# Kernel optimization log

Hardware: AMD Instinct MI355X
Metric: run time of the kernel (lower is better)

Reference implementation:

```python
import jax, jax.numpy as jnp
import numpy as np

T, N, F, H, E = 12, 10000, 32, 64, 320000


def setup_inputs() -> dict:
    key = jax.random.key(0)
    ks = jax.random.split(key, 6)
    x = jax.random.normal(ks[0], (T, N, F), dtype=jnp.float32)
    edge_index = jax.random.randint(ks[1], (2, E), 0, N, dtype=jnp.int64)
    edge_weight = jax.random.uniform(ks[2], (E,), dtype=jnp.float32)
    missing_mask = jnp.ones((T, N, F), dtype=jnp.bool_)
    # GCNConv params (Glorot-ish init); PyG lin: out = x @ W, bias added after aggregation
    W1 = jax.random.normal(ks[3], (F, H), dtype=jnp.float32) * (1.0 / np.sqrt(F))
    b1 = jnp.zeros((H,), dtype=jnp.float32)
    W2 = jax.random.normal(ks[4], (H, F), dtype=jnp.float32) * (1.0 / np.sqrt(H))
    b2 = jnp.zeros((F,), dtype=jnp.float32)
    return dict(x=x, edge_index=edge_index, edge_weight=edge_weight,
                missing_mask=missing_mask, W1=W1, b1=b1, W2=W2, b2=b2)


def _gcn_norm(edge_weight, row, col, n_nodes):
    # PyG gcn_norm with add_self_loops=False: deg from dst, sym normalization
    deg = jax.ops.segment_sum(edge_weight, col, num_segments=n_nodes)
    dinv = jnp.where(deg > 0, 1.0 / jnp.sqrt(jnp.maximum(deg, 1e-12)), 0.0)
    return dinv[row] * edge_weight * dinv[col]


def _gcn_layer(h, row, col, norm, W, b):
    # h: (T, N, Fin) -> (T, N, Fout). Gather at src, weight, scatter-add at dst.
    h = h @ W                                   # (T, N, Fout)
    msg = h[:, row, :] * norm[None, :, None]    # (T, E, Fout)
    out = jnp.zeros((h.shape[0], h.shape[1], h.shape[2]), h.dtype)
    out = out.at[:, col, :].add(msg)
    return out + b


def reference(x, edge_index, edge_weight, missing_mask, W1, b1, W2, b2):
    n_nodes = x.shape[1]
    row, col = edge_index[0], edge_index[1]
    norm = _gcn_norm(edge_weight, row, col, n_nodes)
    h = _gcn_layer(x, row, col, norm, W1, b1)   # layer 0
    h = jax.nn.relu(h)                          # relu between layers
    h = _gcn_layer(h, row, col, norm, W2, b2)   # layer 1 (out_dim = in_dim)
    return jnp.tanh(h)                          # original returns (x, 0); we return x
```

## Files before the change

### kernel.cpp

```cpp
#include <hip/hip_runtime.h>
#include <hip/hip_fp16.h>

#define T_DIM   12
#define N_NODES 10000
#define F_IN    32
#define H_DIM   64
#define NCH     3
#define TC      4
#define CHROW   (TC * F_IN)
#define NGRP    (N_NODES / 16)
#define NTASK   (NCH * NGRP)
#define NROWS   (NCH * N_NODES * TC)
#define MROWS   128

__global__ void zero_kernel(uint4* __restrict__ p, int n16) {
    int i = blockIdx.x * blockDim.x + threadIdx.x;
    if (i < n16) p[i] = make_uint4(0, 0, 0, 0);
}

__global__ void deg_hist_conv_kernel(const int* __restrict__ col,
                                     const float* __restrict__ w,
                                     float* __restrict__ deg,
                                     int* __restrict__ cnt, int E, int eb,
                                     const float* __restrict__ x,
                                     __half* __restrict__ xh) {
    int b = blockIdx.x;
    if (b < eb) {
        int e = b * 256 + threadIdx.x;
        if (e >= E) return;
        int c = col[e];
        atomicAdd(&deg[c], w[e]);
        atomicAdd(&cnt[c], 1);
    } else {
        int task = (b - eb) * 4 + (threadIdx.x >> 6);
        if (task >= NTASK) return;
        int l  = threadIdx.x & 63;
        int ch = task / NGRP;
        int ng = task - ch * NGRP;
        int n  = ng * 16 + (l >> 2);
        int t  = ch * TC + (l & 3);
        const float4* xp = (const float4*)(x + ((size_t)t * N_NODES + n) * F_IN);
        union { uint32_t u[16]; uint4 q[4]; } pk;
#pragma unroll
        for (int i = 0; i < 8; i++) {
            float4 v = xp[i];
            __half2 h0 = __floats2half2_rn(v.x, v.y);
            __half2 h1 = __floats2half2_rn(v.z, v.w);
            pk.u[2 * i]     = *(uint32_t*)&h0;
            pk.u[2 * i + 1] = *(uint32_t*)&h1;
        }
        uint4* dp = (uint4*)(xh + ((size_t)ch * N_NODES * TC + ng * 64 + l) * F_IN);
#pragma unroll
        for (int i = 0; i < 4; i++) dp[i] = pk.q[i];
    }
}

__global__ __launch_bounds__(1024) void scan_kernel(const int* __restrict__ cnt,
                                                    int* __restrict__ rowptr,
                                                    int* __restrict__ cur, int n) {
    __shared__ int part[1024];
    int tid = threadIdx.x;
    const int per = (n + 1023) / 1024;
    int base = tid * per;
    int s = 0;
    for (int i = 0; i < per; i++) {
        int idx = base + i;
        if (idx < n) s += cnt[idx];
    }
    part[tid] = s;
    __syncthreads();
    for (int off = 1; off < 1024; off <<= 1) {
        int v = 0;
        if (tid >= off) v = part[tid - off];
        __syncthreads();
        if (tid >= off) part[tid] += v;
        __syncthreads();
    }
    int run = (tid == 0) ? 0 : part[tid - 1];
    for (int i = 0; i < per; i++) {
        int idx = base + i;
        if (idx < n) { rowptr[idx] = run; cur[idx] = run; run += cnt[idx]; }
    }
    if (tid == 1023) rowptr[n] = part[1023];
}

__global__ void fill_kernel(const int* __restrict__ row,
                            const int* __restrict__ col,
                            const float* __restrict__ w,
                            const float* __restrict__ deg,
                            int* __restrict__ cur,
                            int2* __restrict__ edge_s, int E) {
    int e = blockIdx.x * blockDim.x + threadIdx.x;
    if (e >= E) return;
    int r = row[e];
    int c = col[e];
    float dr = deg[r];
    float dc = deg[c];
    float ir = dr > 0.f ? 1.0f / sqrtf(fmaxf(dr, 1e-12f)) : 0.f;
    float ic = dc > 0.f ? 1.0f / sqrtf(fmaxf(dc, 1e-12f)) : 0.f;
    float nw = ir * w[e] * ic;
    int pos = atomicAdd(&cur[c], 1);
    edge_s[pos] = make_int2(r, __float_as_int(nw));
}

__global__ __launch_bounds__(256) void gather_sp_kernel(const int* __restrict__ rowptr,
                                                        const int2* __restrict__ edge_s,
                                                        const __half* __restrict__ yh,
                                                        float* __restrict__ outp, int n) {
    int c = blockIdx.x * 8 + (threadIdx.x >> 5);
    if (c >= n) return;
    int l = threadIdx.x & 31;

    int beg = rowptr[c], end = rowptr[c + 1];
    const __half* base = yh + 4 * l;
    const size_t cstep = (size_t)N_NODES * CHROW;

    float4 a0 = {0.f, 0.f, 0.f, 0.f};
    float4 a1 = {0.f, 0.f, 0.f, 0.f};
    float4 a2 = {0.f, 0.f, 0.f, 0.f};

#pragma unroll 4
    for (int e = beg; e < end; e++) {
        int2 ed = edge_s[e];
        float nw = __int_as_float(ed.y);
        const __half* p = base + (size_t)ed.x * CHROW;
        uint2 u0 = *(const uint2*)(p);
        uint2 u1 = *(const uint2*)(p + cstep);
        uint2 u2 = *(const uint2*)(p + 2 * cstep);
        float2 f00 = __half22float2(*(__half2*)&u0.x), f01 = __half22float2(*(__half2*)&u0.y);
        float2 f10 = __half22float2(*(__half2*)&u1.x), f11 = __half22float2(*(__half2*)&u1.y);
        float2 f20 = __half22float2(*(__half2*)&u2.x), f21 = __half22float2(*(__half2*)&u2.y);
        a0.x = fmaf(f00.x, nw, a0.x); a0.y = fmaf(f00.y, nw, a0.y);
        a0.z = fmaf(f01.x, nw, a0.z); a0.w = fmaf(f01.y, nw, a0.w);
        a1.x = fmaf(f10.x, nw, a1.x); a1.y = fmaf(f10.y, nw, a1.y);
        a1.z = fmaf(f11.x, nw, a1.z); a1.w = fmaf(f11.y, nw, a1.w);
        a2.x = fmaf(f20.x, nw, a2.x); a2.y = fmaf(f20.y, nw, a2.y);
        a2.z = fmaf(f21.x, nw, a2.z); a2.w = fmaf(f21.y, nw, a2.w);
    }

    float* op = outp + (size_t)c * CHROW + 4 * l;
    const size_t ostep = (size_t)N_NODES * CHROW;
    *(float4*)(op)             = a0;
    *(float4*)(op + ostep)     = a1;
    *(float4*)(op + 2 * ostep) = a2;
}

__global__ __launch_bounds__(256) void gather_ch_kernel(const int* __restrict__ rowptr,
                                                        const int2* __restrict__ edge_s,
                                                        const __half* __restrict__ yh,
                                                        const float* __restrict__ bias,
                                                        float* __restrict__ outp, int n) {
    int c = blockIdx.x * 8 + (threadIdx.x >> 5);
    if (c >= n) return;
    int l = threadIdx.x & 31;

    int beg = rowptr[c], end = rowptr[c + 1];
    float4 b4 = *(const float4*)(bias + 4 * (l & 7));

#pragma unroll
    for (int ch = 0; ch < NCH; ch++) {
        const __half* base = yh + (size_t)ch * N_NODES * CHROW + 4 * l;
        float4 a = {0.f, 0.f, 0.f, 0.f};
#pragma unroll 8
        for (int e = beg; e < end; e++) {
            int2 ed = edge_s[e];
            float nw = __int_as_float(ed.y);
            uint2 u = *(const uint2*)(base + (size_t)ed.x * CHROW);
            float2 f0 = __half22float2(*(__half2*)&u.x);
            float2 f1 = __half22float2(*(__half2*)&u.y);
            a.x = fmaf(f0.x, nw, a.x);
            a.y = fmaf(f0.y, nw, a.y);
            a.z = fmaf(f1.x, nw, a.z);
            a.w = fmaf(f1.y, nw, a.w);
        }
        a.x = tanhf(a.x + b4.x); a.y = tanhf(a.y + b4.y);
        a.z = tanhf(a.z + b4.z); a.w = tanhf(a.w + b4.w);
        float* op = outp + ((size_t)(ch * TC + (l >> 3)) * N_NODES + c) * F_IN + 4 * (l & 7);
        *(float4*)op = a;
    }
}

__global__ __launch_bounds__(128) void mlp_kernel(const float* __restrict__ aggx,
                                                  const float* __restrict__ W1g,
                                                  const float* __restrict__ b1,
                                                  const float* __restrict__ W2g,
                                                  __half* __restrict__ y2h) {
    __shared__ float W1s[F_IN * H_DIM];
    __shared__ float W2s[H_DIM * F_IN];
    __shared__ float b1s[H_DIM];
    __shared__ float xs[MROWS][F_IN + 1];
    __shared__ float hs[MROWS][H_DIM + 1];

    int tid = threadIdx.x;
    for (int i = tid; i < F_IN * H_DIM; i += 128) { W1s[i] = W1g[i]; W2s[i] = W2g[i]; }
    if (tid < H_DIM) b1s[tid] = b1[tid];

    size_t row0 = (size_t)blockIdx.x * MROWS;
    const float4* src = (const float4*)(aggx + row0 * F_IN);
    for (int i = tid; i < MROWS * (F_IN / 4); i += 128) {
        float4 v = src[i];
        int r = i >> 3, q = (i & 7) * 4;
        xs[r][q + 0] = v.x; xs[r][q + 1] = v.y; xs[r][q + 2] = v.z; xs[r][q + 3] = v.w;
    }
    __syncthreads();

    int rg = tid >> 2;
    int cg = tid & 3;
    int r0 = 4 * rg;

    {
        int c0 = 16 * cg;
        float acc[4][16];
#pragma unroll
        for (int j = 0; j < 16; j++) {
            float b = b1s[c0 + j];
#pragma unroll
            for (int rr = 0; rr < 4; rr++) acc[rr][j] = b;
        }
#pragma unroll 8
        for (int k = 0; k < F_IN; k++) {
            float xr[4];
#pragma unroll
            for (int rr = 0; rr < 4; rr++) xr[rr] = xs[r0 + rr][k];
#pragma unroll
            for (int j = 0; j < 16; j++) {
                float wv = W1s[k * H_DIM + c0 + j];
#pragma unroll
                for (int rr = 0; rr < 4; rr++) acc[rr][j] = fmaf(xr[rr], wv, acc[rr][j]);
            }
        }
#pragma unroll
        for (int rr = 0; rr < 4; rr++)
#pragma unroll
            for (int j = 0; j < 16; j++)
                hs[r0 + rr][c0 + j] = fmaxf(acc[rr][j], 0.f);
    }
    __syncthreads();

    {
        int d0 = 8 * cg;
        float acc[4][8];
#pragma unroll
        for (int rr = 0; rr < 4; rr++)
#pragma unroll
            for (int j = 0; j < 8; j++) acc[rr][j] = 0.f;
#pragma unroll 8
        for (int k = 0; k < H_DIM; k++) {
            float hr[4];
#pragma unroll
            for (int rr = 0; rr < 4; rr++) hr[rr] = hs[r0 + rr][k];
#pragma unroll
            for (int j = 0; j < 8; j++) {
                float wv = W2s[k * F_IN + d0 + j];
#pragma unroll
                for (int rr = 0; rr < 4; rr++) acc[rr][j] = fmaf(hr[rr], wv, acc[rr][j]);
            }
        }
#pragma unroll
        for (int rr = 0; rr < 4; rr++) {
            union { uint32_t u[4]; uint4 q; } pk;
#pragma unroll
            for (int i = 0; i < 4; i++) {
                __half2 hh = __floats2half2_rn(acc[rr][2 * i], acc[rr][2 * i + 1]);
                pk.u[i] = *(uint32_t*)&hh;
            }
            *(uint4*)(y2h + (row0 + r0 + rr) * F_IN + d0) = pk.q;
        }
    }
}

extern "C" void kernel_launch(void* const* d_in, const int* in_sizes, int n_in,
                              void* d_out, int out_size, void* d_ws, size_t ws_size,
                              hipStream_t stream) {
    const float* x  = (const float*)d_in[0];
    const int*   ei = (const int*)d_in[1];
    const float* w  = (const float*)d_in[2];
    const float* W1 = (const float*)d_in[4];
    const float* b1 = (const float*)d_in[5];
    const float* W2 = (const float*)d_in[6];
    const float* b2 = (const float*)d_in[7];
    float* out = (float*)d_out;

    const int E = in_sizes[1] / 2;
    const int* row = ei;
    const int* col = ei + E;

    char* ws = (char*)d_ws;
    size_t off = 0;
    auto alloc = [&](size_t bytes) { void* p = ws + off; off += (bytes + 255) & ~(size_t)255; return p; };
    float*  deg    = (float*) alloc(N_NODES * sizeof(float));
    int*    cnt    = (int*)   alloc(N_NODES * sizeof(int));
    int*    cur    = (int*)   alloc(N_NODES * sizeof(int));
    int*    rowptr = (int*)   alloc((N_NODES + 1) * sizeof(int));
    int2*   edge_s = (int2*)  alloc((size_t)E * sizeof(int2));
    __half* xh     = (__half*)alloc((size_t)NROWS * F_IN * sizeof(__half));
    __half* y2h    = (__half*)alloc((size_t)(NROWS + 64) * F_IN * sizeof(__half));
    float*  aggx   = (float*) alloc((size_t)(NROWS + 64) * F_IN * sizeof(float));

    const int eb = (E + 255) / 256;
    const int cb = (NTASK + 3) / 4;
    const int nb = (N_NODES + 7) / 8;
    const int mb = (NROWS + MROWS - 1) / MROWS;

    const int zn = (int)(((char*)(cnt + N_NODES) - (char*)deg) / 16);
    zero_kernel<<<(zn + 255) / 256, 256, 0, stream>>>((uint4*)deg, zn);
    deg_hist_conv_kernel<<<eb + cb, 256, 0, stream>>>(col, w, deg, cnt, E, eb, x, xh);
    scan_kernel<<<1, 1024, 0, stream>>>(cnt, rowptr, cur, N_NODES);
    fill_kernel<<<eb, 256, 0, stream>>>(row, col, w, deg, cur, edge_s, E);

    gather_sp_kernel<<<nb, 256, 0, stream>>>(rowptr, edge_s, xh, aggx, N_NODES);
    mlp_kernel<<<mb, 128, 0, stream>>>(aggx, W1, b1, W2, y2h);

    gather_ch_kernel<<<nb, 256, 0, stream>>>(rowptr, edge_s, y2h, b2, out, N_NODES);
}
```

Measured before the change: 169.8 us.

## Split each node's edge list across two half-wavefronts and share one gather kernel

Replaces the two gather kernels with one templated kernel. Each destination node now gets a full 64-lane wavefront, and the two 32-lane halves process alternating edges before combining their partials with a cross-half shuffle. The second-layer gather now loads all three time-chunks per edge in one pass instead of looping over chunks, which removes repeated edge-list reads. This raises memory-level parallelism per node on a 64-wide wavefront, at the cost of fewer nodes per block and extra shuffle work. The fp32 summation order also changes.

```diff
diff --git a/kernel.cpp b/kernel.cpp
--- a/kernel.cpp
+++ b/kernel.cpp
@@ -103,16 +103,20 @@
     edge_s[pos] = make_int2(r, __float_as_int(nw));
 }
 
-__global__ __launch_bounds__(256) void gather_sp_kernel(const int* __restrict__ rowptr,
-                                                        const int2* __restrict__ edge_s,
-                                                        const __half* __restrict__ yh,
-                                                        float* __restrict__ outp, int n) {
-    int c = blockIdx.x * 8 + (threadIdx.x >> 5);
+template <bool TANH>
+__global__ __launch_bounds__(256) void gather64_kernel(const int* __restrict__ rowptr,
+                                                       const int2* __restrict__ edge_s,
+                                                       const __half* __restrict__ yh,
+                                                       const float* __restrict__ bias,
+                                                       float* __restrict__ outp, int n) {
+    int c = blockIdx.x * 4 + (threadIdx.x >> 6);
     if (c >= n) return;
-    int l = threadIdx.x & 31;
+    int l    = threadIdx.x & 63;
+    int half = l >> 5;
+    int l32  = l & 31;
 
     int beg = rowptr[c], end = rowptr[c + 1];
-    const __half* base = yh + 4 * l;
+    const __half* base = yh + 4 * l32;
     const size_t cstep = (size_t)N_NODES * CHROW;
 
     float4 a0 = {0.f, 0.f, 0.f, 0.f};
@@ -120,7 +124,7 @@
     float4 a2 = {0.f, 0.f, 0.f, 0.f};
 
 #pragma unroll 4
-    for (int e = beg; e < end; e++) {
+    for (int e = beg + half; e < end; e += 2) {
         int2 ed = edge_s[e];
         float nw = __int_as_float(ed.y);
         const __half* p = base + (size_t)ed.x * CHROW;
@@ -138,45 +142,40 @@
         a2.z = fmaf(f21.x, nw, a2.z); a2.w = fmaf(f21.y, nw, a2.w);
     }
 
-    float* op = outp + (size_t)c * CHROW + 4 * l;
-    const size_t ostep = (size_t)N_NODES * CHROW;
-    *(float4*)(op)             = a0;
-    *(float4*)(op + ostep)     = a1;
-    *(float4*)(op + 2 * ostep) = a2;
-}
-
-__global__ __launch_bounds__(256) void gather_ch_kernel(const int* __restrict__ rowptr,
-                                                        const int2* __restrict__ edge_s,
-                                                        const __half* __restrict__ yh,
-                                                        const float* __restrict__ bias,
-                                                        float* __restrict__ outp, int n) {
-    int c = blockIdx.x * 8 + (threadIdx.x >> 5);
-    if (c >= n) return;
-    int l = threadIdx.x & 31;
-
-    int beg = rowptr[c], end = rowptr[c + 1];
-    float4 b4 = *(const float4*)(bias + 4 * (l & 7));
-
-#pragma unroll
-    for (int ch = 0; ch < NCH; ch++) {
-        const __half* base = yh + (size_t)ch * N_NODES * CHROW + 4 * l;
-        float4 a = {0.f, 0.f, 0.f, 0.f};
-#pragma unroll 8
-        for (int e = beg; e < end; e++) {
-            int2 ed = edge_s[e];
-            float nw = __int_as_float(ed.y);
-            uint2 u = *(const uint2*)(base + (size_t)ed.x * CHROW);
-            float2 f0 = __half22float2(*(__half2*)&u.x);
-            float2 f1 = __half22float2(*(__half2*)&u.y);
-            a.x = fmaf(f0.x, nw, a.x);
-            a.y = fmaf(f0.y, nw, a.y);
-            a.z = fmaf(f1.x, nw, a.z);
-            a.w = fmaf(f1.y, nw, a.w);
-        }
-        a.x = tanhf(a.x + b4.x); a.y = tanhf(a.y + b4.y);
-        a.z = tanhf(a.z + b4.z); a.w = tanhf(a.w + b4.w);
-        float* op = outp + ((size_t)(ch * TC + (l >> 3)) * N_NODES + c) * F_IN + 4 * (l & 7);
-        *(float4*)op = a;
+    a0.x += __shfl_xor(a0.x, 32); a0.y += __shfl_xor(a0.y, 32);
+    a0.z += __shfl_xor(a0.z, 32); a0.w += __shfl_xor(a0.w, 32);
+    a1.x += __shfl_xor(a1.x, 32); a1.y += __shfl_xor(a1.y, 32);
+    a1.z += __shfl_xor(a1.z, 32); a1.w += __shfl_xor(a1.w, 32);
+    a2.x += __shfl_xor(a2.x, 32); a2.y += __shfl_xor(a2.y, 32);
+    a2.z += __shfl_xor(a2.z, 32); a2.w += __shfl_xor(a2.w, 32);
+
+    if (TANH) {
+        float4 b4 = *(const float4*)(bias + 4 * (l32 & 7));
+        if (half == 0) {
+            a0.x = tanhf(a0.x + b4.x); a0.y = tanhf(a0.y + b4.y);
+            a0.z = tanhf(a0.z + b4.z); a0.w = tanhf(a0.w + b4.w);
+            a1.x = tanhf(a1.x + b4.x); a1.y = tanhf(a1.y + b4.y);
+            a1.z = tanhf(a1.z + b4.z); a1.w = tanhf(a1.w + b4.w);
+            int t0 = (l32 >> 3);
+            float* op0 = outp + ((size_t)t0 * N_NODES + c) * F_IN + 4 * (l32 & 7);
+            *(float4*)(op0)                              = a0;
+            *(float4*)(op0 + (size_t)TC * N_NODES * F_IN) = a1;
+        } else {
+            a2.x = tanhf(a2.x + b4.x); a2.y = tanhf(a2.y + b4.y);
+            a2.z = tanhf(a2.z + b4.z); a2.w = tanhf(a2.w + b4.w);
+            int t2 = 2 * TC + (l32 >> 3);
+            float* op2 = outp + ((size_t)t2 * N_NODES + c) * F_IN + 4 * (l32 & 7);
+            *(float4*)op2 = a2;
+        }
+    } else {
+        float* op = outp + (size_t)c * CHROW + 4 * l32;
+        const size_t ostep = (size_t)N_NODES * CHROW;
+        if (half == 0) {
+            *(float4*)(op)         = a0;
+            *(float4*)(op + ostep) = a1;
+        } else {
+            *(float4*)(op + 2 * ostep) = a2;
+        }
     }
 }
 
@@ -299,7 +298,7 @@
 
     const int eb = (E + 255) / 256;
     const int cb = (NTASK + 3) / 4;
-    const int nb = (N_NODES + 7) / 8;
+    const int gb = (N_NODES + 3) / 4;
     const int mb = (NROWS + MROWS - 1) / MROWS;
 
     const int zn = (int)(((char*)(cnt + N_NODES) - (char*)deg) / 16);
@@ -308,8 +307,8 @@
     scan_kernel<<<1, 1024, 0, stream>>>(cnt, rowptr, cur, N_NODES);
     fill_kernel<<<eb, 256, 0, stream>>>(row, col, w, deg, cur, edge_s, E);
 
-    gather_sp_kernel<<<nb, 256, 0, stream>>>(rowptr, edge_s, xh, aggx, N_NODES);
+    gather64_kernel<false><<<gb, 256, 0, stream>>>(rowptr, edge_s, xh, nullptr, aggx, N_NODES);
     mlp_kernel<<<mb, 128, 0, stream>>>(aggx, W1, b1, W2, y2h);
 
-    gather_ch_kernel<<<nb, 256, 0, stream>>>(rowptr, edge_s, y2h, b2, out, N_NODES);
-}
+    gather64_kernel<true><<<gb, 256, 0, stream>>>(rowptr, edge_s, y2h, b2, out, N_NODES);
+}
```

Measured after the change: 165.8 us. -2.4%, faster.
